# Kernel tuning notes

Hardware: AMD Instinct MI355X
Metric: run time of the kernel (lower is better)

Reference implementation:

```python
import jax, jax.numpy as jnp
import numpy as np

FACTOR = 0.2          # rotation/zoom/shift factor (init kwarg)
SCALE = 1.0 / 255.0   # rescale (init kwarg)
TWO_PI = 6.283185307179586
B, H, W, C = 64, 224, 224, 3


def _reflect(i, n):
    # TF fill_mode='reflect' index mapping (symmetric with edge repeat)
    m = jnp.mod(i, 2 * n)
    return jnp.where(m >= n, 2 * n - 1 - m, m)


def _bilinear(img, xs, ys):
    # img [H,W,C]; xs, ys [H,W] = input-space sample coords for each output pixel
    h, w, _ = img.shape
    x0f = jnp.floor(xs)
    y0f = jnp.floor(ys)
    fx = (xs - x0f)[..., None]
    fy = (ys - y0f)[..., None]
    x0 = x0f.astype(jnp.int32)
    y0 = y0f.astype(jnp.int32)
    x0r = _reflect(x0, w); x1r = _reflect(x0 + 1, w)
    y0r = _reflect(y0, h); y1r = _reflect(y0 + 1, h)
    Ia = img[y0r, x0r]; Ib = img[y0r, x1r]
    Ic = img[y1r, x0r]; Id = img[y1r, x1r]
    top = Ia * (1.0 - fx) + Ib * fx
    bot = Ic * (1.0 - fx) + Id * fx
    return top * (1.0 - fy) + bot * fy


_warp = jax.vmap(_bilinear)  # over batch: images [B,H,W,C], coords [B,H,W]


def setup_inputs() -> dict:
    key = jax.random.key(0)
    k = jax.random.split(key, 5)
    return {
        "image": jax.random.uniform(k[0], (B, H, W, C), jnp.float32) * 255.0,
        "angle_u": jax.random.uniform(k[1], (B,), jnp.float32),
        "zoom_u": jax.random.uniform(k[2], (B, 2), jnp.float32),
        "shift_u": jax.random.uniform(k[3], (B, 2), jnp.float32),
        "flip_u": jax.random.uniform(k[4], (B,), jnp.float32),
    }


def reference(image, angle_u, zoom_u, shift_u, flip_u):
    b, h, w, _ = image.shape
    dt = image.dtype
    yy, xx = jnp.meshgrid(jnp.arange(h, dtype=dt), jnp.arange(w, dtype=dt), indexing='ij')
    cx = (w - 1) / 2.0
    cy = (h - 1) / 2.0

    # 1) rescale
    x = image * SCALE

    # 2) random rotation: angle uniform in [-factor*2pi, +factor*2pi]
    theta = (2.0 * angle_u - 1.0) * FACTOR * TWO_PI            # [B]
    c = jnp.cos(theta)[:, None, None]
    s = jnp.sin(theta)[:, None, None]
    xr = c * (xx - cx) - s * (yy - cy) + cx                    # [B,H,W]
    yr = s * (xx - cx) + c * (yy - cy) + cy
    x = _warp(x, xr, yr)

    # 3) random zoom: zoom factor uniform in [1-factor, 1+factor] per axis
    z = 1.0 + (2.0 * zoom_u - 1.0) * FACTOR                    # [B,2] (h, w)
    zh = z[:, 0][:, None, None]
    zw = z[:, 1][:, None, None]
    xz = zw * (xx - cx) + cx
    yz = zh * (yy - cy) + cy
    x = _warp(x, xz, yz)

    # 4) random translation: shift fraction uniform in [-factor, factor]
    sh = (2.0 * shift_u - 1.0) * FACTOR                        # [B,2] (h, w)
    dy = (sh[:, 0] * h)[:, None, None]
    dx = (sh[:, 1] * w)[:, None, None]
    xt = xx - dx
    yt = yy - dy
    x = _warp(x, xt, yt)

    # 5) random horizontal flip (p = 0.5)
    flip = flip_u > 0.5
    x = jnp.where(flip[:, None, None, None], x[:, :, ::-1, :], x)
    return x
```

## Files before the change

kernel.cpp:

```cpp
#include <hip/hip_runtime.h>
#include <hip/hip_fp16.h>
#include <math.h>

#define BB 64
#define HH 224
#define WW 224
#define CC 3

constexpr float FACTOR  = 0.2f;
constexpr float SCALE_K = 1.0f / 255.0f;
constexpr float TWO_PI_F = 6.283185307179586f;
constexpr float CX = (WW - 1) * 0.5f;
constexpr float CY = (HH - 1) * 0.5f;
constexpr int PIX = HH * WW;
constexpr int IMG_ELEMS = PIX * CC;

constexpr int TILES_X = WW / 16;
constexpr int TILES_Y = HH / 16;
constexpr int TILES_PER_IMG = TILES_X * TILES_Y;
constexpr int NXCD = 8;
constexpr int NBLOCKS = BB * TILES_PER_IMG;

typedef float f32x4 __attribute__((ext_vector_type(4), aligned(4)));
typedef float f32x2 __attribute__((ext_vector_type(2), aligned(4)));
typedef unsigned int u32x4 __attribute__((ext_vector_type(4), aligned(8)));

__device__ __forceinline__ int reflect1(int i, int n) {
    i = (i < 0) ? (-1 - i) : i;
    return (i >= n) ? (2 * n - 1 - i) : i;
}

__device__ __forceinline__ void decode_tile(int bid, int& b, int& tx, int& ty) {
    int xcd  = bid & (NXCD - 1);
    int slot = bid >> 3;
    int bi   = slot / TILES_PER_IMG;
    int t    = slot - bi * TILES_PER_IMG;
    b = xcd + bi * NXCD;
    ty = t / TILES_X;
    tx = t - ty * TILES_X;
}

__device__ __forceinline__ float h2f(unsigned short u) {
    return __half2float(__ushort_as_half(u));
}

__global__ __launch_bounds__(256)
void rotate_kernel(const float* __restrict__ image, uint2* __restrict__ tmp,
                   const float* __restrict__ angle_u) {
    int b, tx, ty;
    decode_tile(blockIdx.x, b, tx, ty);
    const int x = tx * 16 + (threadIdx.x & 15);
    const int y = ty * 16 + (threadIdx.x >> 4);

    float theta = (2.0f * angle_u[b] - 1.0f) * FACTOR * TWO_PI_F;
    float c = __cosf(theta), s = __sinf(theta);

    float rx = (float)x - CX;
    float ry = (float)y - CY;
    float xs = c * rx - s * ry + CX;
    float ys = s * rx + c * ry + CY;

    float x0f = floorf(xs), y0f = floorf(ys);
    float fx = xs - x0f, fy = ys - y0f;
    int x0 = (int)x0f, y0 = (int)y0f;
    int x0r = reflect1(x0,     WW);
    int x1r = reflect1(x0 + 1, WW);
    int y0r = reflect1(y0,     HH);
    int y1r = reflect1(y0 + 1, HH);

    int xl = min(x0r, x1r); xl = min(xl, WW - 2);
    const bool sA = (x0r != xl);
    const bool sB = (x1r != xl);

    const float* img = image + (size_t)b * IMG_ELEMS;
    const float* rT = img + (y0r * WW + xl) * CC;
    const float* rB = img + (y1r * WW + xl) * CC;

    f32x4 t4 = *(const f32x4*)rT;
    f32x2 t2 = *(const f32x2*)(rT + 4);
    f32x4 b4 = *(const f32x4*)rB;
    f32x2 b2 = *(const f32x2*)(rB + 4);

    float TA[3] = { sA ? t4.w : t4.x, sA ? t2.x : t4.y, sA ? t2.y : t4.z };
    float TB[3] = { sB ? t4.w : t4.x, sB ? t2.x : t4.y, sB ? t2.y : t4.z };
    float BA[3] = { sA ? b4.w : b4.x, sA ? b2.x : b4.y, sA ? b2.y : b4.z };
    float BC[3] = { sB ? b4.w : b4.x, sB ? b2.x : b4.y, sB ? b2.y : b4.z };

    const float omfx = 1.0f - fx;
    const float omfy = 1.0f - fy;

    float o[3];
#pragma unroll
    for (int ch = 0; ch < CC; ++ch) {
        float top = TA[ch] * omfx + TB[ch] * fx;
        float bot = BA[ch] * omfx + BC[ch] * fx;
        o[ch] = (top * omfy + bot * fy) * SCALE_K;
    }

    unsigned u0 = __half_as_ushort(__float2half_rn(o[0]));
    unsigned u1 = __half_as_ushort(__float2half_rn(o[1]));
    unsigned u2 = __half_as_ushort(__float2half_rn(o[2]));
    uint2 v;
    v.x = u0 | (u1 << 16);
    v.y = u2;
    tmp[(size_t)b * PIX + y * WW + x] = v;
}

__global__ __launch_bounds__(256)
void zoomshift_kernel(const uint2* __restrict__ tmp, float* __restrict__ out,
                      const float* __restrict__ zoom_u,
                      const float* __restrict__ shift_u,
                      const float* __restrict__ flip_u) {
    int b, tx, ty;
    decode_tile(blockIdx.x, b, tx, ty);

    const float zh = 1.0f + (2.0f * zoom_u[2 * b + 0] - 1.0f) * FACTOR;
    const float zw = 1.0f + (2.0f * zoom_u[2 * b + 1] - 1.0f) * FACTOR;
    const float dy = ((2.0f * shift_u[2 * b + 0] - 1.0f) * FACTOR) * (float)HH;
    const float dx = ((2.0f * shift_u[2 * b + 1] - 1.0f) * FACTOR) * (float)WW;
    const bool flip = flip_u[b] > 0.5f;

    const float ndxf = floorf(-dx), ndyf = floorf(-dy);
    const int Kx = (int)ndxf, Ky = (int)ndyf;
    const float fx3 = -dx - ndxf;
    const float fy3 = -dy - ndyf;

    const int Xmin = (flip ? (WW - 16 - tx * 16) : tx * 16) + Kx;
    const int Ymin = ty * 16 + Ky;

    __shared__ float Z[17 * 17 * 3];

    const uint2* img = tmp + (size_t)b * PIX;

    for (int e = threadIdx.x; e < 17 * 17; e += 256) {
        int ey = e / 17;
        int ex = e - ey * 17;
        int Yr = reflect1(Ymin + ey, HH);
        int Xr = reflect1(Xmin + ex, WW);

        float ys2 = zh * ((float)Yr - CY) + CY;
        float xs2 = zw * ((float)Xr - CX) + CX;
        float yf = floorf(ys2), xf = floorf(xs2);
        float fy2 = ys2 - yf, fx2 = xs2 - xf;
        int y20 = (int)yf, x20 = (int)xf;
        int r0 = reflect1(y20,     HH);
        int r1 = reflect1(y20 + 1, HH);
        int c0 = reflect1(x20,     WW);
        int c1 = reflect1(x20 + 1, WW);

        int cl = min(c0, c1); cl = min(cl, WW - 2);
        const bool sA = (c0 != cl);
        const bool sB = (c1 != cl);

        u32x4 vT = *(const u32x4*)(img + r0 * WW + cl);
        u32x4 vB = *(const u32x4*)(img + r1 * WW + cl);

        unsigned aT0 = sA ? vT.z : vT.x, aT1 = sA ? vT.w : vT.y;
        unsigned bT0 = sB ? vT.z : vT.x, bT1 = sB ? vT.w : vT.y;
        unsigned aB0 = sA ? vB.z : vB.x, aB1 = sA ? vB.w : vB.y;
        unsigned bB0 = sB ? vB.z : vB.x, bB1 = sB ? vB.w : vB.y;

        float A[3] = { h2f((unsigned short)(aT0 & 0xffffu)),
                       h2f((unsigned short)(aT0 >> 16)),
                       h2f((unsigned short)(aT1 & 0xffffu)) };
        float Bv[3] = { h2f((unsigned short)(bT0 & 0xffffu)),
                        h2f((unsigned short)(bT0 >> 16)),
                        h2f((unsigned short)(bT1 & 0xffffu)) };
        float Cv[3] = { h2f((unsigned short)(aB0 & 0xffffu)),
                        h2f((unsigned short)(aB0 >> 16)),
                        h2f((unsigned short)(aB1 & 0xffffu)) };
        float Dv[3] = { h2f((unsigned short)(bB0 & 0xffffu)),
                        h2f((unsigned short)(bB0 >> 16)),
                        h2f((unsigned short)(bB1 & 0xffffu)) };

        const float omfx = 1.0f - fx2, omfy = 1.0f - fy2;
        float* zp = &Z[e * 3];
#pragma unroll
        for (int ch = 0; ch < CC; ++ch) {
            float top = A[ch]  * omfx + Bv[ch] * fx2;
            float bot = Cv[ch] * omfx + Dv[ch] * fx2;
            zp[ch] = top * omfy + bot * fy2;
        }
    }
    __syncthreads();

    const int lx = threadIdx.x & 15, ly = threadIdx.x >> 4;
    const int x = tx * 16 + lx, y = ty * 16 + ly;
    const int ix = flip ? (15 - lx) : lx;
    const int iy = ly;

    const float* z00 = &Z[(iy * 17 + ix) * 3];
    const float* z01 = &Z[(iy * 17 + ix + 1) * 3];
    const float* z10 = &Z[((iy + 1) * 17 + ix) * 3];
    const float* z11 = &Z[((iy + 1) * 17 + ix + 1) * 3];

    float* o = out + ((size_t)b * PIX + (size_t)y * WW + x) * CC;
    const float omfx3 = 1.0f - fx3, omfy3 = 1.0f - fy3;
#pragma unroll
    for (int ch = 0; ch < CC; ++ch) {
        float top = z00[ch] * omfx3 + z01[ch] * fx3;
        float bot = z10[ch] * omfx3 + z11[ch] * fx3;
        o[ch] = top * omfy3 + bot * fy3;
    }
}

extern "C" void kernel_launch(void* const* d_in, const int* in_sizes, int n_in,
                              void* d_out, int out_size, void* d_ws, size_t ws_size,
                              hipStream_t stream) {
    const float* image   = (const float*)d_in[0];
    const float* angle_u = (const float*)d_in[1];
    const float* zoom_u  = (const float*)d_in[2];
    const float* shift_u = (const float*)d_in[3];
    const float* flip_u  = (const float*)d_in[4];
    float* out = (float*)d_out;

    uint2* tmp = (uint2*)d_ws;

    rotate_kernel<<<NBLOCKS, 256, 0, stream>>>(image, tmp, angle_u);
    zoomshift_kernel<<<NBLOCKS, 256, 0, stream>>>(tmp, out, zoom_u, shift_u, flip_u);
}
```

Baseline: 37.88 us.

## Stage zoom source rectangle in LDS and use 32x16 tiles for zoom-shift

The zoom-shift kernel now processes 32x16 output tiles. It computes the reflected bounding box of the source pixels the zoom needs and cooperatively loads that 24x48 fp16 patch from the intermediate buffer into shared memory. Per-column and per-row sample indices and weights are precomputed once into small LDS tables, and the 17x33 zoom grid is then interpolated from LDS instead of issuing scattered global gathers per element. This reduces redundant global loads and index math. In exchange it uses more LDS, adds an extra barrier, and relies on the patch bounds (clamped to 24x48) covering every sample.

Result: faster. 36.57 us (-3.4%).

```diff
diff --git a/kernel.cpp b/kernel.cpp
--- a/kernel.cpp
+++ b/kernel.cpp
@@ -16,10 +16,17 @@
 constexpr int IMG_ELEMS = PIX * CC;
 
 constexpr int TILES_X = WW / 16;
-constexpr int TILES_Y = HH / 16;
-constexpr int TILES_PER_IMG = TILES_X * TILES_Y;
+constexpr int TILES_PER_IMG = TILES_X * TILES_X;
 constexpr int NXCD = 8;
 constexpr int NBLOCKS = BB * TILES_PER_IMG;
+
+constexpr int T2X = WW / 32;
+constexpr int T2Y = HH / 16;
+constexpr int TILES2 = T2X * T2Y;
+constexpr int NBLOCKS2 = BB * TILES2;
+
+constexpr int SZP = 50;
+constexpr int ZP2 = 34;
 
 typedef float f32x4 __attribute__((ext_vector_type(4), aligned(4)));
 typedef float f32x2 __attribute__((ext_vector_type(2), aligned(4)));
@@ -30,7 +37,18 @@
     return (i >= n) ? (2 * n - 1 - i) : i;
 }
 
-__device__ __forceinline__ void decode_tile(int bid, int& b, int& tx, int& ty) {
+__device__ __forceinline__ void rhull(int a, int b, int n, int& lo, int& hi) {
+    int ra = reflect1(a, n), rb = reflect1(b, n);
+    lo = min(ra, rb); hi = max(ra, rb);
+    if (a <= 0 && b >= -1) lo = 0;
+    if (b >= n - 1 && a <= n) hi = n - 1;
+}
+
+__device__ __forceinline__ float h2f(unsigned short u) {
+    return __half2float(__ushort_as_half(u));
+}
+
+__device__ __forceinline__ void decode_tile16(int bid, int& b, int& tx, int& ty) {
     int xcd  = bid & (NXCD - 1);
     int slot = bid >> 3;
     int bi   = slot / TILES_PER_IMG;
@@ -40,15 +58,11 @@
     tx = t - ty * TILES_X;
 }
 
-__device__ __forceinline__ float h2f(unsigned short u) {
-    return __half2float(__ushort_as_half(u));
-}
-
 __global__ __launch_bounds__(256)
 void rotate_kernel(const float* __restrict__ image, uint2* __restrict__ tmp,
                    const float* __restrict__ angle_u) {
     int b, tx, ty;
-    decode_tile(blockIdx.x, b, tx, ty);
+    decode_tile16(blockIdx.x, b, tx, ty);
     const int x = tx * 16 + (threadIdx.x & 15);
     const int y = ty * 16 + (threadIdx.x >> 4);
 
@@ -111,8 +125,19 @@
                       const float* __restrict__ zoom_u,
                       const float* __restrict__ shift_u,
                       const float* __restrict__ flip_u) {
-    int b, tx, ty;
-    decode_tile(blockIdx.x, b, tx, ty);
+    __shared__ uint2  Sz[24 * SZP];
+    __shared__ float4 Z[17 * ZP2];
+    __shared__ float4 XD[33], YD[17];
+
+    const int tid = threadIdx.x;
+    const int xcd  = blockIdx.x & (NXCD - 1);
+    const int slot = blockIdx.x >> 3;
+    const int bi   = slot / TILES2;
+    const int t    = slot - bi * TILES2;
+    const int b    = xcd + bi * NXCD;
+    const int ty   = t / T2X;
+    const int tx   = t - ty * T2X;
+    const int ox = tx * 32, oy = ty * 16;
 
     const float zh = 1.0f + (2.0f * zoom_u[2 * b + 0] - 1.0f) * FACTOR;
     const float zw = 1.0f + (2.0f * zoom_u[2 * b + 1] - 1.0f) * FACTOR;
@@ -122,85 +147,91 @@
 
     const float ndxf = floorf(-dx), ndyf = floorf(-dy);
     const int Kx = (int)ndxf, Ky = (int)ndyf;
-    const float fx3 = -dx - ndxf;
-    const float fy3 = -dy - ndyf;
-
-    const int Xmin = (flip ? (WW - 16 - tx * 16) : tx * 16) + Kx;
-    const int Ymin = ty * 16 + Ky;
-
-    __shared__ float Z[17 * 17 * 3];
-
-    const uint2* img = tmp + (size_t)b * PIX;
-
-    for (int e = threadIdx.x; e < 17 * 17; e += 256) {
-        int ey = e / 17;
-        int ex = e - ey * 17;
-        int Yr = reflect1(Ymin + ey, HH);
-        int Xr = reflect1(Xmin + ex, WW);
-
-        float ys2 = zh * ((float)Yr - CY) + CY;
-        float xs2 = zw * ((float)Xr - CX) + CX;
-        float yf = floorf(ys2), xf = floorf(xs2);
-        float fy2 = ys2 - yf, fx2 = xs2 - xf;
-        int y20 = (int)yf, x20 = (int)xf;
-        int r0 = reflect1(y20,     HH);
-        int r1 = reflect1(y20 + 1, HH);
-        int c0 = reflect1(x20,     WW);
-        int c1 = reflect1(x20 + 1, WW);
-
-        int cl = min(c0, c1); cl = min(cl, WW - 2);
-        const bool sA = (c0 != cl);
-        const bool sB = (c1 != cl);
-
-        u32x4 vT = *(const u32x4*)(img + r0 * WW + cl);
-        u32x4 vB = *(const u32x4*)(img + r1 * WW + cl);
-
-        unsigned aT0 = sA ? vT.z : vT.x, aT1 = sA ? vT.w : vT.y;
-        unsigned bT0 = sB ? vT.z : vT.x, bT1 = sB ? vT.w : vT.y;
-        unsigned aB0 = sA ? vB.z : vB.x, aB1 = sA ? vB.w : vB.y;
-        unsigned bB0 = sB ? vB.z : vB.x, bB1 = sB ? vB.w : vB.y;
-
-        float A[3] = { h2f((unsigned short)(aT0 & 0xffffu)),
-                       h2f((unsigned short)(aT0 >> 16)),
-                       h2f((unsigned short)(aT1 & 0xffffu)) };
-        float Bv[3] = { h2f((unsigned short)(bT0 & 0xffffu)),
-                        h2f((unsigned short)(bT0 >> 16)),
-                        h2f((unsigned short)(bT1 & 0xffffu)) };
-        float Cv[3] = { h2f((unsigned short)(aB0 & 0xffffu)),
-                        h2f((unsigned short)(aB0 >> 16)),
-                        h2f((unsigned short)(aB1 & 0xffffu)) };
-        float Dv[3] = { h2f((unsigned short)(bB0 & 0xffffu)),
-                        h2f((unsigned short)(bB0 >> 16)),
-                        h2f((unsigned short)(bB1 & 0xffffu)) };
-
-        const float omfx = 1.0f - fx2, omfy = 1.0f - fy2;
-        float* zp = &Z[e * 3];
+    const float fx3 = -dx - ndxf, fy3 = -dy - ndyf;
+
+    const int Xmin = (flip ? WW - 32 - ox : ox) + Kx;
+    const int Ymin = oy + Ky;
+
+    int XrLo, XrHi, YrLo, YrHi;
+    rhull(Xmin, Xmin + 32, WW, XrLo, XrHi);
+    rhull(Ymin, Ymin + 16, HH, YrLo, YrHi);
+    const int Gx0 = (int)floorf(zw * ((float)XrLo - CX) + CX);
+    const int Gx1 = (int)floorf(zw * ((float)XrHi - CX) + CX) + 1;
+    const int Gy0 = (int)floorf(zh * ((float)YrLo - CY) + CY);
+    const int Gy1 = (int)floorf(zh * ((float)YrHi - CY) + CY) + 1;
+    int Cx0, Cx1, Cy0, Cy1;
+    rhull(Gx0, Gx1, WW, Cx0, Cx1);
+    rhull(Gy0, Gy1, HH, Cy0, Cy1);
+    const int ColBase = max(min(Cx0, WW - 48), 0) & ~1;
+    const int RowBase = max(min(Cy0, HH - 24), 0);
+
+    const uint2* timg = tmp + (size_t)b * PIX;
+    for (int id = tid; id < 576; id += 256) {
+        const int row = id / 24;
+        const int g   = id - row * 24;
+        u32x4 v = *(const u32x4*)(timg + (size_t)(RowBase + row) * WW + ColBase + g * 2);
+        *(u32x4*)(&Sz[row * SZP + g * 2]) = v;
+    }
+
+    if (tid < 33) {
+        const int Xr = reflect1(Xmin + tid, WW);
+        const float xs2 = zw * ((float)Xr - CX) + CX;
+        const float xf = floorf(xs2);
+        const int x20 = (int)xf;
+        const int cA = min(max(reflect1(x20,     WW) - ColBase, 0), 47);
+        const int cB = min(max(reflect1(x20 + 1, WW) - ColBase, 0), 47);
+        XD[tid] = make_float4(xs2 - xf, __int_as_float(cA), __int_as_float(cB), 0.f);
+    } else if (tid >= 64 && tid < 81) {
+        const int ey = tid - 64;
+        const int Yr = reflect1(Ymin + ey, HH);
+        const float ys2 = zh * ((float)Yr - CY) + CY;
+        const float yf = floorf(ys2);
+        const int y20 = (int)yf;
+        const int rA = min(max(reflect1(y20,     HH) - RowBase, 0), 23) * SZP;
+        const int rB = min(max(reflect1(y20 + 1, HH) - RowBase, 0), 23) * SZP;
+        YD[ey] = make_float4(ys2 - yf, __int_as_float(rA), __int_as_float(rB), 0.f);
+    }
+    __syncthreads();
+
+    for (int e = tid; e < 17 * 33; e += 256) {
+        const int ey = e / 33;
+        const int ex = e - ey * 33;
+        const float4 xd = XD[ex];
+        const float4 yd = YD[ey];
+        const int cA = __float_as_int(xd.y), cB = __float_as_int(xd.z);
+        const int rA = __float_as_int(yd.y), rB = __float_as_int(yd.z);
+        const uint2 va = Sz[rA + cA];
+        const uint2 vb = Sz[rA + cB];
+        const uint2 vc = Sz[rB + cA];
+        const uint2 vd = Sz[rB + cB];
+        const float fx2 = xd.x, fy2 = yd.x;
+        const float ofx = 1.0f - fx2, ofy = 1.0f - fy2;
+        float4 res;
+        res.x = (h2f((unsigned short)(va.x & 0xffffu)) * ofx + h2f((unsigned short)(vb.x & 0xffffu)) * fx2) * ofy
+              + (h2f((unsigned short)(vc.x & 0xffffu)) * ofx + h2f((unsigned short)(vd.x & 0xffffu)) * fx2) * fy2;
+        res.y = (h2f((unsigned short)(va.x >> 16)) * ofx + h2f((unsigned short)(vb.x >> 16)) * fx2) * ofy
+              + (h2f((unsigned short)(vc.x >> 16)) * ofx + h2f((unsigned short)(vd.x >> 16)) * fx2) * fy2;
+        res.z = (h2f((unsigned short)(va.y & 0xffffu)) * ofx + h2f((unsigned short)(vb.y & 0xffffu)) * fx2) * ofy
+              + (h2f((unsigned short)(vc.y & 0xffffu)) * ofx + h2f((unsigned short)(vd.y & 0xffffu)) * fx2) * fy2;
+        res.w = 0.f;
+        Z[ey * ZP2 + ex] = res;
+    }
+    __syncthreads();
+
+    const float ofx = 1.0f - fx3, ofy = 1.0f - fy3;
 #pragma unroll
-        for (int ch = 0; ch < CC; ++ch) {
-            float top = A[ch]  * omfx + Bv[ch] * fx2;
-            float bot = Cv[ch] * omfx + Dv[ch] * fx2;
-            zp[ch] = top * omfy + bot * fy2;
-        }
-    }
-    __syncthreads();
-
-    const int lx = threadIdx.x & 15, ly = threadIdx.x >> 4;
-    const int x = tx * 16 + lx, y = ty * 16 + ly;
-    const int ix = flip ? (15 - lx) : lx;
-    const int iy = ly;
-
-    const float* z00 = &Z[(iy * 17 + ix) * 3];
-    const float* z01 = &Z[(iy * 17 + ix + 1) * 3];
-    const float* z10 = &Z[((iy + 1) * 17 + ix) * 3];
-    const float* z11 = &Z[((iy + 1) * 17 + ix + 1) * 3];
-
-    float* o = out + ((size_t)b * PIX + (size_t)y * WW + x) * CC;
-    const float omfx3 = 1.0f - fx3, omfy3 = 1.0f - fy3;
-#pragma unroll
-    for (int ch = 0; ch < CC; ++ch) {
-        float top = z00[ch] * omfx3 + z01[ch] * fx3;
-        float bot = z10[ch] * omfx3 + z11[ch] * fx3;
-        o[ch] = top * omfy3 + bot * fy3;
+    for (int i = 0; i < 2; ++i) {
+        const int p  = tid + 256 * i;
+        const int lx = p & 31, ly = p >> 5;
+        const int ix = flip ? (31 - lx) : lx;
+        const float4 A  = Z[ly * ZP2 + ix];
+        const float4 Bv = Z[ly * ZP2 + ix + 1];
+        const float4 Cv = Z[(ly + 1) * ZP2 + ix];
+        const float4 Dv = Z[(ly + 1) * ZP2 + ix + 1];
+        float* o = out + ((size_t)b * PIX + (size_t)(oy + ly) * WW + (ox + lx)) * CC;
+        o[0] = (A.x * ofx + Bv.x * fx3) * ofy + (Cv.x * ofx + Dv.x * fx3) * fy3;
+        o[1] = (A.y * ofx + Bv.y * fx3) * ofy + (Cv.y * ofx + Dv.y * fx3) * fy3;
+        o[2] = (A.z * ofx + Bv.z * fx3) * ofy + (Cv.z * ofx + Dv.z * fx3) * fy3;
     }
 }
 
@@ -217,5 +248,5 @@
     uint2* tmp = (uint2*)d_ws;
 
     rotate_kernel<<<NBLOCKS, 256, 0, stream>>>(image, tmp, angle_u);
-    zoomshift_kernel<<<NBLOCKS, 256, 0, stream>>>(tmp, out, zoom_u, shift_u, flip_u);
-}
+    zoomshift_kernel<<<NBLOCKS2, 256, 0, stream>>>(tmp, out, zoom_u, shift_u, flip_u);
+}
```
